# Kernel optimization log

Hardware: AMD Instinct MI355X
Metric: run time of the kernel (lower is better)

The kernel has to match this reference:

```python
import jax, jax.numpy as jnp
import numpy as np

N = 100_000   # nodes
E = 1_600_000 # edges (avg degree 16)
D = 128       # feature dim (input = hidden = output = mlp hidden)
L = 3         # GIN layers
EPS = 0.0     # init_eps, not learned


def setup_inputs() -> dict:
    key = jax.random.key(0)
    ks = jax.random.split(key, 7)
    feat = jax.random.normal(ks[0], (N, D), jnp.float32)
    # scale weights ~ 1/sqrt(fan_in) for numerically sane activations
    W1 = jax.random.normal(ks[1], (L, D, D), jnp.float32) / np.float32(np.sqrt(D))
    b1 = jax.random.normal(ks[2], (L, D), jnp.float32) * 0.01
    W2 = jax.random.normal(ks[3], (L, D, D), jnp.float32) / np.float32(np.sqrt(D))
    b2 = jax.random.normal(ks[4], (L, D), jnp.float32) * 0.01
    src = jax.random.randint(ks[5], (E,), 0, N, dtype=jnp.int32)
    dst = jax.random.randint(ks[6], (E,), 0, N, dtype=jnp.int32)
    return {"feat": feat, "W1": W1, "b1": b1, "W2": W2, "b2": b2,
            "src": src, "dst": dst}


def reference(feat, W1, b1, W2, b2, src, dst):
    h = feat
    for i in range(L):
        # sum-aggregate neighbor (source) features into destination nodes
        neigh = jax.ops.segment_sum(h[src], dst, num_segments=N)  # [N, D]
        rst = (1.0 + EPS) * h + neigh
        # 2-layer MLP: hidden layer uses act+norm(none), last layer is plain linear
        if i < L - 1:
            h1 = jax.nn.relu(rst @ W1[i] + b1[i])
            h2 = h1 @ W2[i] + b2[i]
            h = jax.nn.relu(h2)  # ApplyNodeFunc: norm(none) -> relu
        else:
            # last GIN layer: activation 'none' everywhere
            h1 = rst @ W1[i] + b1[i]
            h = h1 @ W2[i] + b2[i]
    return h
```

## Files before the change

kernel.cpp:

```cpp
#include <hip/hip_runtime.h>
#include <hip/hip_bf16.h>

#define D 128
#define NBUCK_SHIFT 9
#define PAD_SLACK 2048

typedef __bf16 bf16x8 __attribute__((ext_vector_type(8)));
typedef float f32x4 __attribute__((ext_vector_type(4)));
typedef float f32x2 __attribute__((ext_vector_type(2)));
typedef int i32x4 __attribute__((ext_vector_type(4)));
typedef int i32x2 __attribute__((ext_vector_type(2)));
typedef unsigned int u32x4 __attribute__((ext_vector_type(4)));
typedef unsigned short u16x4_t __attribute__((ext_vector_type(4)));
typedef unsigned short u16x8_t __attribute__((ext_vector_type(8)));

__device__ __forceinline__ unsigned short f2b(float f) {
    __hip_bfloat16 h = __float2bfloat16(f);
    return __builtin_bit_cast(unsigned short, h);
}

__device__ __forceinline__ void acc8(f32x2* acc, u32x4 x) {
#pragma unroll
    for (int r = 0; r < 4; ++r) {
        f32x2 t;
        t[0] = __builtin_bit_cast(float, x[r] << 16);
        t[1] = __builtin_bit_cast(float, x[r] & 0xffff0000u);
        acc[r] += t;
    }
}

__global__ __launch_bounds__(256) void prep_kernel(
        const float4* __restrict__ feat4, ushort4* __restrict__ outA, int n4,
        const float* __restrict__ W1, const float* __restrict__ W2,
        unsigned short* __restrict__ W1L, unsigned short* __restrict__ W2L, int wtotal,
        int* __restrict__ bco, unsigned short* __restrict__ bufA,
        unsigned short* __restrict__ bufB, int N) {
    int b = blockIdx.x;
    int t = threadIdx.x;
    int nCast = (n4 + 255) >> 8;
    int nW = (wtotal + 255) >> 8;
    if (b < nCast) {
        int i = b * 256 + t;
        if (i < n4) {
            float4 f = feat4[i];
            ushort4 o;
            o.x = f2b(f.x); o.y = f2b(f.y); o.z = f2b(f.z); o.w = f2b(f.w);
            outA[i] = o;
        }
    } else if (b < nCast + nW) {
        int i = (b - nCast) * 256 + t;
        if (i < wtotal) {
            int l = i >> 14;
            int rem = i & 16383;
            int k = rem >> 7;
            int n = rem & 127;
            int nt = n >> 4, l15 = n & 15;
            int kb = k >> 5, lg = (k >> 3) & 3, j = k & 7;
            int o = ((l * 32 + nt * 4 + kb) * 64 + lg * 16 + l15) * 8 + j;
            W1L[o] = f2b(W1[i]);
            W2L[o] = f2b(W2[i]);
        }
    } else {
        bco[t] = 0;
        bco[t + 256] = 0;
        if (t < 128) {
            bufA[(size_t)N * D + t] = 0;
            bufB[(size_t)N * D + t] = 0;
        }
    }
}

__global__ __launch_bounds__(256) void coarse_hist_kernel(
        const int* __restrict__ dst, int* __restrict__ bco, int E, int nbuck) {
    __shared__ int s[256];
    int t = threadIdx.x;
    s[t] = 0;
    __syncthreads();
    for (int i = blockIdx.x * 256 + t; i < E; i += gridDim.x * 256)
        atomicAdd(&s[dst[i] >> NBUCK_SHIFT], 1);
    __syncthreads();
    if (t < nbuck && s[t] > 0) atomicAdd(&bco[t], s[t]);
}

__global__ __launch_bounds__(256) void bucket_kernel(
        const int* __restrict__ src, const int* __restrict__ dst,
        const int* __restrict__ bco, int* __restrict__ bcursor,
        unsigned int* __restrict__ pairs, int E, int nbuck) {
    __shared__ int lcnt[256];
    __shared__ int lbase[256];
    int t = threadIdx.x;
    int base = blockIdx.x * 4096;
    int c0 = bco[t];
    lbase[t] = c0;
    __syncthreads();
    for (int o = 1; o < 256; o <<= 1) {
        int y = (t >= o) ? lbase[t - o] : 0;
        __syncthreads();
        lbase[t] += y;
        __syncthreads();
    }
    int ebase = lbase[t] - c0;
    __syncthreads();
    if (t < nbuck) lcnt[t] = 0;
    __syncthreads();
    int d[16], s[16];
#pragma unroll
    for (int k = 0; k < 16; ++k) {
        int i = base + t + k * 256;
        if (i < E) {
            d[k] = dst[i];
            s[k] = src[i];
            atomicAdd(&lcnt[d[k] >> NBUCK_SHIFT], 1);
        } else {
            d[k] = -1;
            s[k] = 0;
        }
    }
    __syncthreads();
    if (t < nbuck) {
        int c = lcnt[t];
        int g = (c > 0) ? atomicAdd(&bcursor[t], c) : 0;
        lbase[t] = ebase + g;
        lcnt[t] = 0;
    }
    __syncthreads();
#pragma unroll
    for (int k = 0; k < 16; ++k) {
        if (d[k] >= 0) {
            int b = d[k] >> NBUCK_SHIFT;
            int r = atomicAdd(&lcnt[b], 1);
            pairs[lbase[b] + r] = ((unsigned)s[k] << 9) | ((unsigned)d[k] & 511u);
        }
    }
}

__global__ __launch_bounds__(1024) void bucket_build_kernel(
        const unsigned int* __restrict__ pairs, const int* __restrict__ bco,
        i32x2* __restrict__ rowse, int* __restrict__ col, int* __restrict__ rowhead,
        int N, int E) {
    __shared__ int cnt[512];
    __shared__ int off[512];
    __shared__ int s01[2];
    int t = threadIdx.x;
    int b = blockIdx.x;
    if (t < 256) off[t] = bco[t];
    __syncthreads();
    for (int o = 1; o < 256; o <<= 1) {
        int y = (t < 256 && t >= o) ? off[t - o] : 0;
        __syncthreads();
        if (t < 256) off[t] += y;
        __syncthreads();
    }
    if (t == 0) {
        s01[1] = off[b];
        s01[0] = off[b] - bco[b];
    }
    __syncthreads();
    int s0 = s01[0], s1 = s01[1];
    int p0 = ((s0 + 3) & ~3) + b * PAD_SLACK;
    if (t < 512) cnt[t] = 0;
    __syncthreads();
    for (int i = s0 + t; i < s1; i += 1024)
        atomicAdd(&cnt[pairs[i] & 511u], 1);
    __syncthreads();
    int deg = (t < 512) ? cnt[t] : 0;
    int ovp = (deg > 15) ? ((deg - 15 + 3) & ~3) : 0;
    if (t < 512) off[t] = ovp;
    __syncthreads();
    for (int o = 1; o < 512; o <<= 1) {
        int y = (t < 512 && t >= o) ? off[t - o] : 0;
        __syncthreads();
        if (t < 512) off[t] += y;
        __syncthreads();
    }
    int v0 = b << NBUCK_SHIFT;
    int zoff = N << 8;
    if (t < 512) {
        int ex = off[t] - ovp;
        off[t] = ex;
        cnt[t] = 0;
        int v = v0 + t;
        if (v < N) {
            i32x2 se;
            se[0] = p0 + ex;
            se[1] = p0 + ex + ovp;
            rowse[v] = se;
            int* rhv = rowhead + (size_t)v * 16;
            rhv[0] = v << 8;
            int ninl = deg < 15 ? deg : 15;
            for (int q = 1 + ninl; q < 16; ++q) rhv[q] = zoff;
        }
    }
    __syncthreads();
    for (int i = s0 + t; i < s1; i += 1024) {
        unsigned int p = pairs[i];
        int li = (int)(p & 511u);
        int x = (int)(p >> 9);
        int s = atomicAdd(&cnt[li], 1);
        if (s < 15) rowhead[(size_t)(v0 + li) * 16 + 1 + s] = x << 8;
        else        col[p0 + off[li] + (s - 15)] = x << 8;
    }
    __syncthreads();
    if (t < 512) {
        int cc = cnt[t];
        int ovreal = (cc > 15) ? cc - 15 : 0;
        int base2 = p0 + off[t];
        int endp = base2 + ((ovreal + 3) & ~3);
        for (int q = base2 + ovreal; q < endp; ++q) col[q] = zoff;
    }
}

#define RSTRIDE 136
__global__ __launch_bounds__(256, 4) void fused_kernel(
        const unsigned short* __restrict__ h, const i32x2* __restrict__ rowse,
        const int* __restrict__ col, const i32x4* __restrict__ rowhead,
        const unsigned short* __restrict__ W1L, const unsigned short* __restrict__ W2L,
        const float* __restrict__ b1, const float* __restrict__ b2,
        unsigned short* __restrict__ hOut, float* __restrict__ fOut,
        int mode, int ntiles, int N) {
    __shared__ float b1s[128], b2s[128];
    __shared__ unsigned short rstile[16 * RSTRIDE];
    __shared__ unsigned short h1buf[2560];
    int tid = threadIdx.x;
    if (tid < 128) b1s[tid] = b1[tid];
    else b2s[tid - 128] = b2[tid - 128];
    int wave = tid >> 6, lane = tid & 63;
    int v0 = blockIdx.x << 4;

    {
        int i = lane & 15;
        int j = lane >> 4;
        const char* __restrict__ hb = (const char*)h;
        unsigned ioff = (unsigned)i * 16u;
        for (int q = 0; q < 4; ++q) {
            int m = wave * 4 + q;
            int v = v0 + m;
            f32x2 accA[4], accB[4], accC[4], accD[4];
#pragma unroll
            for (int r = 0; r < 4; ++r) {
                accA[r] = (f32x2){0.f, 0.f};
                accB[r] = (f32x2){0.f, 0.f};
                accC[r] = (f32x2){0.f, 0.f};
                accD[r] = (f32x2){0.f, 0.f};
            }
            if (v < N) {
                i32x4 c4 = __builtin_nontemporal_load(&rowhead[(size_t)v * 4 + j]);
                i32x2 se = __builtin_nontemporal_load(&rowse[v]);
                u32x4 x0 = *(const u32x4*)(hb + ((unsigned)c4[0] + ioff));
                u32x4 x1 = *(const u32x4*)(hb + ((unsigned)c4[1] + ioff));
                u32x4 x2 = *(const u32x4*)(hb + ((unsigned)c4[2] + ioff));
                u32x4 x3 = *(const u32x4*)(hb + ((unsigned)c4[3] + ioff));
                int e = se[0] + 4 * j;
                int e1 = se[1];
                bool have = (e < e1);
                i32x4 o4;
                if (have) o4 = __builtin_nontemporal_load((const i32x4*)(col + e));
                acc8(accA, x0);
                acc8(accB, x1);
                acc8(accC, x2);
                acc8(accD, x3);
                while (have) {
                    int en = e + 16;
                    bool haven = (en < e1);
                    i32x4 o4n;
                    if (haven) o4n = __builtin_nontemporal_load((const i32x4*)(col + en));
                    u32x4 y0 = *(const u32x4*)(hb + ((unsigned)o4[0] + ioff));
                    u32x4 y1 = *(const u32x4*)(hb + ((unsigned)o4[1] + ioff));
                    u32x4 y2 = *(const u32x4*)(hb + ((unsigned)o4[2] + ioff));
                    u32x4 y3 = *(const u32x4*)(hb + ((unsigned)o4[3] + ioff));
                    acc8(accA, y0);
                    acc8(accB, y1);
                    acc8(accC, y2);
                    acc8(accD, y3);
                    o4 = o4n;
                    e = en;
                    have = haven;
                }
            }
            unsigned short outv[8];
#pragma unroll
            for (int r = 0; r < 4; ++r) {
                f32x2 s = (accA[r] + accB[r]) + (accC[r] + accD[r]);
                float lo = s[0], hi = s[1];
                lo += __shfl_xor(lo, 16);
                lo += __shfl_xor(lo, 32);
                hi += __shfl_xor(hi, 16);
                hi += __shfl_xor(hi, 32);
                outv[2 * r] = f2b(lo);
                outv[2 * r + 1] = f2b(hi);
            }
            if (j == 0) {
                u16x8_t o;
#pragma unroll
                for (int r = 0; r < 8; ++r) o[r] = outv[r];
                *(u16x8_t*)(rstile + m * RSTRIDE + i * 8) = o;
            }
        }
    }
    __syncthreads();

    int l15 = lane & 15, lg = lane >> 4;
    bf16x8 bfrag[4];
#pragma unroll
    for (int kb = 0; kb < 4; ++kb)
        bfrag[kb] = *(const bf16x8*)(rstile + l15 * RSTRIDE + lg * 8 + kb * 32);

    f32x4 acc[2];
#pragma unroll
    for (int t = 0; t < 2; ++t) acc[t] = (f32x4){0.f, 0.f, 0.f, 0.f};
#pragma unroll
    for (int kb = 0; kb < 4; ++kb)
#pragma unroll
        for (int t = 0; t < 2; ++t) {
            int nt = wave * 2 + t;
            bf16x8 wf = *(const bf16x8*)(W1L + ((nt * 4 + kb) * 64 + lane) * 8);
            acc[t] = __builtin_amdgcn_mfma_f32_16x16x32_bf16(wf, bfrag[kb], acc[t], 0, 0, 0);
        }
#pragma unroll
    for (int t = 0; t < 2; ++t) {
        int nt = wave * 2 + t;
        f32x4 bias = *(const f32x4*)(b1s + nt * 16 + lg * 4);
        int kb2 = nt >> 1;
        int lgk = (nt & 1) * 2 + (lg >> 1);
        int U = kb2 * 80 + l15 * 5 + lgk;
        u16x4_t o;
#pragma unroll
        for (int r = 0; r < 4; ++r) {
            float x = acc[t][r] + bias[r];
            if (mode == 0) x = fmaxf(x, 0.f);
            o[r] = f2b(x);
        }
        *(u16x4_t*)(h1buf + U * 8 + (lg & 1) * 4) = o;
    }
    __syncthreads();
    bf16x8 bf2[4];
#pragma unroll
    for (int kb = 0; kb < 4; ++kb)
        bf2[kb] = *(const bf16x8*)(h1buf + (kb * 80 + l15 * 5 + lg) * 8);
#pragma unroll
    for (int t = 0; t < 2; ++t) acc[t] = (f32x4){0.f, 0.f, 0.f, 0.f};
#pragma unroll
    for (int kb = 0; kb < 4; ++kb)
#pragma unroll
        for (int t = 0; t < 2; ++t) {
            int nt = wave * 2 + t;
            bf16x8 wf = *(const bf16x8*)(W2L + ((nt * 4 + kb) * 64 + lane) * 8);
            acc[t] = __builtin_amdgcn_mfma_f32_16x16x32_bf16(wf, bf2[kb], acc[t], 0, 0, 0);
        }
    int m = v0 + l15;
    if (m < N) {
#pragma unroll
        for (int t = 0; t < 2; ++t) {
            int nt = wave * 2 + t;
            f32x4 bias = *(const f32x4*)(b2s + nt * 16 + lg * 4);
            int c0 = nt * 16 + lg * 4;
            if (mode == 0) {
                u16x4_t o;
#pragma unroll
                for (int r = 0; r < 4; ++r) o[r] = f2b(fmaxf(acc[t][r] + bias[r], 0.f));
                *(u16x4_t*)(hOut + (size_t)m * D + c0) = o;
            } else {
                f32x4 o;
#pragma unroll
                for (int r = 0; r < 4; ++r) o[r] = acc[t][r] + bias[r];
                *(f32x4*)(fOut + (size_t)m * D + c0) = o;
            }
        }
    }
}

extern "C" void kernel_launch(void* const* d_in, const int* in_sizes, int n_in,
                              void* d_out, int out_size, void* d_ws, size_t ws_size,
                              hipStream_t stream) {
    const float* feat = (const float*)d_in[0];
    const float* W1 = (const float*)d_in[1];
    const float* b1 = (const float*)d_in[2];
    const float* W2 = (const float*)d_in[3];
    const float* b2 = (const float*)d_in[4];
    const int* src = (const int*)d_in[5];
    const int* dst = (const int*)d_in[6];

    const int N = in_sizes[0] / D;
    const int L = in_sizes[2] / D;
    const int E = in_sizes[5];

    char* w = (char*)d_ws;
    size_t off = 0;
    auto alloc = [&](size_t bytes) {
        void* p = w + off;
        off = (off + bytes + 255) & ~(size_t)255;
        return p;
    };
    unsigned short* bufA = (unsigned short*)alloc((size_t)(N + 1) * D * 2);
    unsigned short* bufB = (unsigned short*)alloc((size_t)(N + 1) * D * 2);
    unsigned int* pairs = (unsigned int*)alloc((size_t)E * 4);
    int* col = (int*)alloc(((size_t)E + 256 * PAD_SLACK + 16) * 4);
    int* rowhead = (int*)alloc((size_t)N * 16 * 4);
    i32x2* rowse = (i32x2*)alloc((size_t)N * 8);
    int* bco = (int*)alloc(512 * 4);
    int* bcursor = bco + 256;
    unsigned short* W1L = (unsigned short*)alloc((size_t)L * 16384 * 2);
    unsigned short* W2L = (unsigned short*)alloc((size_t)L * 16384 * 2);

    int nbuck = (N + (1 << NBUCK_SHIFT) - 1) >> NBUCK_SHIFT;

    int n4 = N * D / 4;
    int wtotal = L * D * D;
    int nCast = (n4 + 255) / 256;
    int nW = (wtotal + 255) / 256;
    prep_kernel<<<nCast + nW + 1, 256, 0, stream>>>(
        (const float4*)feat, (ushort4*)bufA, n4, W1, W2, W1L, W2L, wtotal,
        bco, bufA, bufB, N);
    coarse_hist_kernel<<<512, 256, 0, stream>>>(dst, bco, E, nbuck);
    bucket_kernel<<<(E + 4095) / 4096, 256, 0, stream>>>(src, dst, bco, bcursor, pairs, E, nbuck);
    bucket_build_kernel<<<nbuck, 1024, 0, stream>>>(pairs, bco, rowse, col, rowhead, N, E);

    int ntiles = (N + 15) / 16;
    const unsigned short* hin[3] = {bufA, bufB, bufA};
    unsigned short* hout[3] = {bufB, bufA, nullptr};
    for (int i = 0; i < L; ++i) {
        int mode = (i == L - 1) ? 1 : 0;
        fused_kernel<<<ntiles, 256, 0, stream>>>(hin[i], rowse, col, (const i32x4*)rowhead,
                                                 W1L + (size_t)i * 16384, W2L + (size_t)i * 16384,
                                                 b1 + i * D, b2 + i * D, hout[i], (float*)d_out,
                                                 mode, ntiles, N);
    }
}
```

Baseline: 390.1 us.

## Fold coarse histogram into prep kernel and precompute per-node degrees

Removes the separate coarse_hist kernel launch by running the bucket histogram inside extra blocks of prep_kernel. Those blocks also count per-node degrees with global atomics, so bucket_build_kernel no longer makes a counting pass over its pairs. Zeroing of bco and deg moves to hipMemsetAsync calls. In exchange it adds 1.6M global atomics on the deg array and two memset operations, which may cost more than the launch and the pass it removes.

```diff
diff --git a/kernel.cpp b/kernel.cpp
--- a/kernel.cpp
+++ b/kernel.cpp
@@ -33,8 +33,10 @@
         const float4* __restrict__ feat4, ushort4* __restrict__ outA, int n4,
         const float* __restrict__ W1, const float* __restrict__ W2,
         unsigned short* __restrict__ W1L, unsigned short* __restrict__ W2L, int wtotal,
-        int* __restrict__ bco, unsigned short* __restrict__ bufA,
-        unsigned short* __restrict__ bufB, int N) {
+        const int* __restrict__ dst, int E,
+        int* __restrict__ bco, int* __restrict__ deg,
+        unsigned short* __restrict__ bufA, unsigned short* __restrict__ bufB, int N) {
+    __shared__ int s[256];
     int b = blockIdx.x;
     int t = threadIdx.x;
     int nCast = (n4 + 255) >> 8;
@@ -60,26 +62,26 @@
             W1L[o] = f2b(W1[i]);
             W2L[o] = f2b(W2[i]);
         }
+    } else if (b < nCast + nW + 512) {
+        int hb = b - nCast - nW;
+        s[t] = 0;
+        __syncthreads();
+        int chunk = (E + 511) >> 9;
+        int lo = hb * chunk;
+        int hi = lo + chunk; if (hi > E) hi = E;
+        for (int i = lo + t; i < hi; i += 256) {
+            int d = dst[i];
+            atomicAdd(&s[d >> NBUCK_SHIFT], 1);
+            atomicAdd(&deg[d], 1);
+        }
+        __syncthreads();
+        if (s[t] > 0) atomicAdd(&bco[t], s[t]);
     } else {
-        bco[t] = 0;
-        bco[t + 256] = 0;
         if (t < 128) {
             bufA[(size_t)N * D + t] = 0;
             bufB[(size_t)N * D + t] = 0;
         }
     }
-}
-
-__global__ __launch_bounds__(256) void coarse_hist_kernel(
-        const int* __restrict__ dst, int* __restrict__ bco, int E, int nbuck) {
-    __shared__ int s[256];
-    int t = threadIdx.x;
-    s[t] = 0;
-    __syncthreads();
-    for (int i = blockIdx.x * 256 + t; i < E; i += gridDim.x * 256)
-        atomicAdd(&s[dst[i] >> NBUCK_SHIFT], 1);
-    __syncthreads();
-    if (t < nbuck && s[t] > 0) atomicAdd(&bco[t], s[t]);
 }
 
 __global__ __launch_bounds__(256) void bucket_kernel(
@@ -136,6 +138,7 @@
 
 __global__ __launch_bounds__(1024) void bucket_build_kernel(
         const unsigned int* __restrict__ pairs, const int* __restrict__ bco,
+        const int* __restrict__ deg,
         i32x2* __restrict__ rowse, int* __restrict__ col, int* __restrict__ rowhead,
         int N, int E) {
     __shared__ int cnt[512];
@@ -158,13 +161,10 @@
     __syncthreads();
     int s0 = s01[0], s1 = s01[1];
     int p0 = ((s0 + 3) & ~3) + b * PAD_SLACK;
-    if (t < 512) cnt[t] = 0;
-    __syncthreads();
-    for (int i = s0 + t; i < s1; i += 1024)
-        atomicAdd(&cnt[pairs[i] & 511u], 1);
-    __syncthreads();
-    int deg = (t < 512) ? cnt[t] : 0;
-    int ovp = (deg > 15) ? ((deg - 15 + 3) & ~3) : 0;
+    int v0 = b << NBUCK_SHIFT;
+    int v = v0 + t;
+    int dg = (t < 512 && v < N) ? deg[v] : 0;
+    int ovp = (dg > 15) ? ((dg - 15 + 3) & ~3) : 0;
     if (t < 512) off[t] = ovp;
     __syncthreads();
     for (int o = 1; o < 512; o <<= 1) {
@@ -173,13 +173,11 @@
         if (t < 512) off[t] += y;
         __syncthreads();
     }
-    int v0 = b << NBUCK_SHIFT;
     int zoff = N << 8;
     if (t < 512) {
         int ex = off[t] - ovp;
         off[t] = ex;
         cnt[t] = 0;
-        int v = v0 + t;
         if (v < N) {
             i32x2 se;
             se[0] = p0 + ex;
@@ -187,7 +185,7 @@
             rowse[v] = se;
             int* rhv = rowhead + (size_t)v * 16;
             rhv[0] = v << 8;
-            int ninl = deg < 15 ? deg : 15;
+            int ninl = dg < 15 ? dg : 15;
             for (int q = 1 + ninl; q < 16; ++q) rhv[q] = zoff;
         }
     }
@@ -202,8 +200,7 @@
     }
     __syncthreads();
     if (t < 512) {
-        int cc = cnt[t];
-        int ovreal = (cc > 15) ? cc - 15 : 0;
+        int ovreal = (dg > 15) ? dg - 15 : 0;
         int base2 = p0 + off[t];
         int endp = base2 + ((ovreal + 3) & ~3);
         for (int q = base2 + ovreal; q < endp; ++q) col[q] = zoff;
@@ -397,6 +394,7 @@
     int* col = (int*)alloc(((size_t)E + 256 * PAD_SLACK + 16) * 4);
     int* rowhead = (int*)alloc((size_t)N * 16 * 4);
     i32x2* rowse = (i32x2*)alloc((size_t)N * 8);
+    int* deg = (int*)alloc((size_t)N * 4);
     int* bco = (int*)alloc(512 * 4);
     int* bcursor = bco + 256;
     unsigned short* W1L = (unsigned short*)alloc((size_t)L * 16384 * 2);
@@ -404,16 +402,17 @@
 
     int nbuck = (N + (1 << NBUCK_SHIFT) - 1) >> NBUCK_SHIFT;
 
+    hipMemsetAsync(bco, 0, 512 * 4, stream);
+    hipMemsetAsync(deg, 0, (size_t)N * 4, stream);
     int n4 = N * D / 4;
     int wtotal = L * D * D;
     int nCast = (n4 + 255) / 256;
     int nW = (wtotal + 255) / 256;
-    prep_kernel<<<nCast + nW + 1, 256, 0, stream>>>(
+    prep_kernel<<<nCast + nW + 512 + 1, 256, 0, stream>>>(
         (const float4*)feat, (ushort4*)bufA, n4, W1, W2, W1L, W2L, wtotal,
-        bco, bufA, bufB, N);
-    coarse_hist_kernel<<<512, 256, 0, stream>>>(dst, bco, E, nbuck);
+        dst, E, bco, deg, bufA, bufB, N);
     bucket_kernel<<<(E + 4095) / 4096, 256, 0, stream>>>(src, dst, bco, bcursor, pairs, E, nbuck);
-    bucket_build_kernel<<<nbuck, 1024, 0, stream>>>(pairs, bco, rowse, col, rowhead, N, E);
+    bucket_build_kernel<<<nbuck, 1024, 0, stream>>>(pairs, bco, deg, rowse, col, rowhead, N, E);
 
     int ntiles = (N + 15) / 16;
     const unsigned short* hin[3] = {bufA, bufB, bufA};
```

New measurement: 464.9 us. 1.19x slower.

## Process 64 nodes per block and keep MLP weight fragments in registers

Applied to the files above, without the earlier changes.

Each block of the fused GIN layer kernel now aggregates 64 nodes instead of 16, with every wave gathering 16 nodes into its own LDS tile. The W1 and W2 MFMA fragments are loaded into registers once per block and reused across four 16-row tiles, which cuts repeated weight fetches and per-block setup (bias loads, launch count). In exchange, register pressure rises from holding 16 weight fragments, LDS use grows, each tile now pays extra barriers, and the grid has a quarter as many blocks, which can reduce latency hiding in the gather phase.

```diff
diff --git a/kernel.cpp b/kernel.cpp
--- a/kernel.cpp
+++ b/kernel.cpp
@@ -219,22 +219,21 @@
         unsigned short* __restrict__ hOut, float* __restrict__ fOut,
         int mode, int ntiles, int N) {
     __shared__ float b1s[128], b2s[128];
-    __shared__ unsigned short rstile[16 * RSTRIDE];
+    __shared__ unsigned short rstile[4][16 * RSTRIDE];
     __shared__ unsigned short h1buf[2560];
     int tid = threadIdx.x;
     if (tid < 128) b1s[tid] = b1[tid];
     else b2s[tid - 128] = b2[tid - 128];
     int wave = tid >> 6, lane = tid & 63;
-    int v0 = blockIdx.x << 4;
+    int v0 = blockIdx.x << 6;
 
     {
         int i = lane & 15;
         int j = lane >> 4;
         const char* __restrict__ hb = (const char*)h;
         unsigned ioff = (unsigned)i * 16u;
-        for (int q = 0; q < 4; ++q) {
-            int m = wave * 4 + q;
-            int v = v0 + m;
+        for (int q = 0; q < 16; ++q) {
+            int v = v0 + wave * 16 + q;
             f32x2 accA[4], accB[4], accC[4], accD[4];
 #pragma unroll
             for (int r = 0; r < 4; ++r) {
@@ -293,79 +292,87 @@
                 u16x8_t o;
 #pragma unroll
                 for (int r = 0; r < 8; ++r) o[r] = outv[r];
-                *(u16x8_t*)(rstile + m * RSTRIDE + i * 8) = o;
+                *(u16x8_t*)(rstile[wave] + q * RSTRIDE + i * 8) = o;
             }
         }
     }
     __syncthreads();
 
     int l15 = lane & 15, lg = lane >> 4;
-    bf16x8 bfrag[4];
-#pragma unroll
-    for (int kb = 0; kb < 4; ++kb)
-        bfrag[kb] = *(const bf16x8*)(rstile + l15 * RSTRIDE + lg * 8 + kb * 32);
-
-    f32x4 acc[2];
-#pragma unroll
-    for (int t = 0; t < 2; ++t) acc[t] = (f32x4){0.f, 0.f, 0.f, 0.f};
-#pragma unroll
-    for (int kb = 0; kb < 4; ++kb)
+    bf16x8 w1f[2][4], w2f[2][4];
+#pragma unroll
+    for (int t = 0; t < 2; ++t) {
+        int nt = wave * 2 + t;
+#pragma unroll
+        for (int kb = 0; kb < 4; ++kb) {
+            w1f[t][kb] = *(const bf16x8*)(W1L + ((nt * 4 + kb) * 64 + lane) * 8);
+            w2f[t][kb] = *(const bf16x8*)(W2L + ((nt * 4 + kb) * 64 + lane) * 8);
+        }
+    }
+
+    for (int tt = 0; tt < 4; ++tt) {
+        bf16x8 bfrag[4];
+#pragma unroll
+        for (int kb = 0; kb < 4; ++kb)
+            bfrag[kb] = *(const bf16x8*)(rstile[tt] + l15 * RSTRIDE + lg * 8 + kb * 32);
+
+        f32x4 acc[2];
+#pragma unroll
+        for (int t = 0; t < 2; ++t) acc[t] = (f32x4){0.f, 0.f, 0.f, 0.f};
+#pragma unroll
+        for (int kb = 0; kb < 4; ++kb)
+#pragma unroll
+            for (int t = 0; t < 2; ++t)
+                acc[t] = __builtin_amdgcn_mfma_f32_16x16x32_bf16(w1f[t][kb], bfrag[kb], acc[t], 0, 0, 0);
 #pragma unroll
         for (int t = 0; t < 2; ++t) {
             int nt = wave * 2 + t;
-            bf16x8 wf = *(const bf16x8*)(W1L + ((nt * 4 + kb) * 64 + lane) * 8);
-            acc[t] = __builtin_amdgcn_mfma_f32_16x16x32_bf16(wf, bfrag[kb], acc[t], 0, 0, 0);
-        }
-#pragma unroll
-    for (int t = 0; t < 2; ++t) {
-        int nt = wave * 2 + t;
-        f32x4 bias = *(const f32x4*)(b1s + nt * 16 + lg * 4);
-        int kb2 = nt >> 1;
-        int lgk = (nt & 1) * 2 + (lg >> 1);
-        int U = kb2 * 80 + l15 * 5 + lgk;
-        u16x4_t o;
-#pragma unroll
-        for (int r = 0; r < 4; ++r) {
-            float x = acc[t][r] + bias[r];
-            if (mode == 0) x = fmaxf(x, 0.f);
-            o[r] = f2b(x);
-        }
-        *(u16x4_t*)(h1buf + U * 8 + (lg & 1) * 4) = o;
-    }
-    __syncthreads();
-    bf16x8 bf2[4];
-#pragma unroll
-    for (int kb = 0; kb < 4; ++kb)
-        bf2[kb] = *(const bf16x8*)(h1buf + (kb * 80 + l15 * 5 + lg) * 8);
-#pragma unroll
-    for (int t = 0; t < 2; ++t) acc[t] = (f32x4){0.f, 0.f, 0.f, 0.f};
-#pragma unroll
-    for (int kb = 0; kb < 4; ++kb)
-#pragma unroll
-        for (int t = 0; t < 2; ++t) {
-            int nt = wave * 2 + t;
-            bf16x8 wf = *(const bf16x8*)(W2L + ((nt * 4 + kb) * 64 + lane) * 8);
-            acc[t] = __builtin_amdgcn_mfma_f32_16x16x32_bf16(wf, bf2[kb], acc[t], 0, 0, 0);
-        }
-    int m = v0 + l15;
-    if (m < N) {
-#pragma unroll
-        for (int t = 0; t < 2; ++t) {
-            int nt = wave * 2 + t;
-            f32x4 bias = *(const f32x4*)(b2s + nt * 16 + lg * 4);
-            int c0 = nt * 16 + lg * 4;
-            if (mode == 0) {
-                u16x4_t o;
-#pragma unroll
-                for (int r = 0; r < 4; ++r) o[r] = f2b(fmaxf(acc[t][r] + bias[r], 0.f));
-                *(u16x4_t*)(hOut + (size_t)m * D + c0) = o;
-            } else {
-                f32x4 o;
-#pragma unroll
-                for (int r = 0; r < 4; ++r) o[r] = acc[t][r] + bias[r];
-                *(f32x4*)(fOut + (size_t)m * D + c0) = o;
-            }
-        }
+            f32x4 bias = *(const f32x4*)(b1s + nt * 16 + lg * 4);
+            int kb2 = nt >> 1;
+            int lgk = (nt & 1) * 2 + (lg >> 1);
+            int U = kb2 * 80 + l15 * 5 + lgk;
+            u16x4_t o;
+#pragma unroll
+            for (int r = 0; r < 4; ++r) {
+                float x = acc[t][r] + bias[r];
+                if (mode == 0) x = fmaxf(x, 0.f);
+                o[r] = f2b(x);
+            }
+            *(u16x4_t*)(h1buf + U * 8 + (lg & 1) * 4) = o;
+        }
+        __syncthreads();
+        bf16x8 bf2[4];
+#pragma unroll
+        for (int kb = 0; kb < 4; ++kb)
+            bf2[kb] = *(const bf16x8*)(h1buf + (kb * 80 + l15 * 5 + lg) * 8);
+#pragma unroll
+        for (int t = 0; t < 2; ++t) acc[t] = (f32x4){0.f, 0.f, 0.f, 0.f};
+#pragma unroll
+        for (int kb = 0; kb < 4; ++kb)
+#pragma unroll
+            for (int t = 0; t < 2; ++t)
+                acc[t] = __builtin_amdgcn_mfma_f32_16x16x32_bf16(w2f[t][kb], bf2[kb], acc[t], 0, 0, 0);
+        int m = v0 + tt * 16 + l15;
+        if (m < N) {
+#pragma unroll
+            for (int t = 0; t < 2; ++t) {
+                int nt = wave * 2 + t;
+                f32x4 bias = *(const f32x4*)(b2s + nt * 16 + lg * 4);
+                int c0 = nt * 16 + lg * 4;
+                if (mode == 0) {
+                    u16x4_t o;
+#pragma unroll
+                    for (int r = 0; r < 4; ++r) o[r] = f2b(fmaxf(acc[t][r] + bias[r], 0.f));
+                    *(u16x4_t*)(hOut + (size_t)m * D + c0) = o;
+                } else {
+                    f32x4 o;
+#pragma unroll
+                    for (int r = 0; r < 4; ++r) o[r] = acc[t][r] + bias[r];
+                    *(f32x4*)(fOut + (size_t)m * D + c0) = o;
+                }
+            }
+        }
+        __syncthreads();
     }
 }
 
@@ -416,13 +423,14 @@
     bucket_build_kernel<<<nbuck, 1024, 0, stream>>>(pairs, bco, rowse, col, rowhead, N, E);
 
     int ntiles = (N + 15) / 16;
+    int fgrid = (N + 63) / 64;
     const unsigned short* hin[3] = {bufA, bufB, bufA};
     unsigned short* hout[3] = {bufB, bufA, nullptr};
     for (int i = 0; i < L; ++i) {
         int mode = (i == L - 1) ? 1 : 0;
-        fused_kernel<<<ntiles, 256, 0, stream>>>(hin[i], rowse, col, (const i32x4*)rowhead,
-                                                 W1L + (size_t)i * 16384, W2L + (size_t)i * 16384,
-                                                 b1 + i * D, b2 + i * D, hout[i], (float*)d_out,
-                                                 mode, ntiles, N);
-    }
-}
+        fused_kernel<<<fgrid, 256, 0, stream>>>(hin[i], rowse, col, (const i32x4*)rowhead,
+                                                W1L + (size_t)i * 16384, W2L + (size_t)i * 16384,
+                                                b1 + i * D, b2 + i * D, hout[i], (float*)d_out,
+                                                mode, ntiles, N);
+    }
+}
```

Result: slower. 404.7 us (+3.8%).
